# Kernel tuning notes

Measured on AMD Instinct MI355X. Metric: run time of the kernel, lower is better.

The kernel has to match this reference:

```python
import jax, jax.numpy as jnp
import numpy as np

TEMPERATURE = 0.07
HARD_NEG_WEIGHT = 0.5
MARGIN = 0.2
NUM_HARD_NEG = 3
BATCH = 8192
DIM = 256
NUM_CLASSES = 512


def setup_inputs() -> dict:
    key = jax.random.key(0)
    k1, k2 = jax.random.split(key)
    embeddings = jax.random.normal(k1, (BATCH, DIM), dtype=jnp.float32)
    labels = jax.random.randint(k2, (BATCH,), 0, NUM_CLASSES, dtype=jnp.int64)
    return {"embeddings": embeddings, "labels": labels}


def reference(embeddings, labels):
    B = embeddings.shape[0]
    dt = embeddings.dtype
    # L2 normalize (torch F.normalize with eps clamp)
    norm = jnp.maximum(jnp.linalg.norm(embeddings, axis=-1, keepdims=True), 1e-12)
    e = embeddings / norm
    sim = jnp.matmul(e, e.T) / TEMPERATURE  # [B, B]

    same = (labels[:, None] == labels[None, :]).astype(dt)
    eye = jnp.eye(B, dtype=dt)
    pos_mask = same - eye            # positives excluding self
    neg_mask = 1.0 - same            # negatives (diag is 0 since labels==labels)

    # basic InfoNCE-style loss (unnormalized exp, as in the original)
    exp_sim = jnp.exp(sim) * (1.0 - eye)
    pos_sim = (exp_sim * pos_mask).sum(axis=-1)
    all_sim = exp_sim.sum(axis=-1)
    basic = -jnp.log(pos_sim / (all_sim + 1e-10) + 1e-10)
    has_pos = pos_mask.sum(axis=-1) > 0
    hp = has_pos.astype(dt)
    n_hp = jnp.maximum(hp.sum(), 1.0)
    basic_loss = (basic * hp).sum() / n_hp

    # hard negative mining: top-k most similar negatives vs best positive
    neg_inf = -jnp.inf
    neg_sim = jnp.where(neg_mask > 0, sim, neg_inf)
    k = min(NUM_HARD_NEG, B - 1)
    hard_neg_mean = jax.lax.top_k(neg_sim, k)[0].mean(axis=-1)
    pos_max = jnp.where(pos_mask > 0, sim, neg_inf).max(axis=-1)
    h = jax.nn.relu(hard_neg_mean - pos_max + MARGIN)
    h = jnp.where(has_pos, h, 0.0)
    hard_loss = (h * hp).sum() / n_hp

    # margin ranking: max positive vs max negative
    max_neg = neg_sim.max(axis=-1)
    m = jax.nn.relu(max_neg - pos_max + MARGIN)
    valid = (pos_max > neg_inf) & (max_neg > neg_inf)
    v = valid.astype(dt)
    n_v = jnp.maximum(v.sum(), 1.0)
    margin_loss = jnp.where(v.sum() > 0, jnp.where(valid, m, 0.0).sum() / n_v, 0.0)

    total = basic_loss + HARD_NEG_WEIGHT * hard_loss + 0.1 * margin_loss
    return total
```

## Files before the change

kernel.cpp:

```cpp
#include <hip/hip_runtime.h>
#include <cstdint>
#include <cstddef>

#define BATCH  8192
#define DIM    256
#define NSTRIP 8
#define SCOLS  1024
#define MROWS  128
#define NTILE  64
#define NITER  (SCOLS/NTILE)

static constexpr float INV_T   = 1.0f / 0.07f;
static constexpr float EXP2_SC = 1.4426950408889634f / 0.07f;
static constexpr float MARGIN  = 0.2f;

typedef __attribute__((ext_vector_type(8))) short short8;
typedef __attribute__((ext_vector_type(4))) float f32x4;

__device__ __forceinline__ unsigned short f2bf(float f){
  unsigned int u = __float_as_uint(f);
  u += 0x7FFFu + ((u >> 16) & 1u);
  return (unsigned short)(u >> 16);
}

__device__ __forceinline__ void ins3(float& t0, float& t1, float& t2, float s){
  float m0 = fmaxf(t0, s); float r1 = fminf(t0, s); t0 = m0;
  float m1 = fmaxf(t1, r1); float r2 = fminf(t1, r1); t1 = m1;
  t2 = fmaxf(t2, r2);
}

__global__ void norm_cast_kernel(const float* __restrict__ emb,
                                 unsigned short* __restrict__ E,
                                 float* __restrict__ accum){
  if (blockIdx.x == 0 && threadIdx.x < 8) accum[threadIdx.x] = 0.0f;
  const int wave = threadIdx.x >> 6;
  const int lane = threadIdx.x & 63;
  const int row  = blockIdx.x * 4 + wave;
  const float4 v = *(const float4*)(emb + (size_t)row * DIM + lane * 4);
  float ss = v.x*v.x + v.y*v.y + v.z*v.z + v.w*v.w;
  #pragma unroll
  for (int m = 1; m < 64; m <<= 1) ss += __shfl_xor(ss, m, 64);
  float nrm = fmaxf(sqrtf(ss), 1e-12f);
  float inv = 1.0f / nrm;
  ushort4 o;
  o.x = f2bf(v.x * inv); o.y = f2bf(v.y * inv);
  o.z = f2bf(v.z * inv); o.w = f2bf(v.w * inv);
  *(ushort4*)(E + (size_t)row * DIM + lane * 4) = o;
}

__global__ __launch_bounds__(256, 2)
void sim_stats_kernel(const unsigned short* __restrict__ E,
                      const int* __restrict__ labels,
                      float* __restrict__ partials){
  const int strip = blockIdx.x;
  const int rb    = blockIdx.y * MROWS;
  const int cs    = strip * SCOLS;
  const int tid   = threadIdx.x;
  const int wave  = tid >> 6;
  const int lane  = tid & 63;
  const int l     = lane & 15;
  const int q     = lane >> 4;

  __shared__ short8 Bs[32 * 64];
  __shared__ int labs[SCOLS];

  for (int i = tid; i < SCOLS; i += 256) labs[i] = labels[cs + i];

  const int row0 = rb + wave * 32;

  short8 a[2][8];
  #pragma unroll
  for (int rt = 0; rt < 2; ++rt){
    const unsigned short* rp = E + (size_t)(row0 + rt*16 + l) * DIM + q * 8;
    #pragma unroll
    for (int kk = 0; kk < 8; ++kk)
      a[rt][kk] = *(const short8*)(rp + kk * 32);
  }

  int labr[2][4];
  #pragma unroll
  for (int rt = 0; rt < 2; ++rt)
    #pragma unroll
    for (int rr = 0; rr < 4; ++rr)
      labr[rt][rr] = labels[row0 + rt*16 + q*4 + rr];

  float all_s[8], pos_s[8], pos_m[8], t0[8], t1[8], t2[8];
  #pragma unroll
  for (int s = 0; s < 8; ++s){
    all_s[s] = 0.f; pos_s[s] = 0.f;
    pos_m[s] = -INFINITY; t0[s] = -INFINITY; t1[s] = -INFINITY; t2[s] = -INFINITY;
  }

  for (int it = 0; it < NITER; ++it){
    const int cb = cs + it * NTILE;
    __syncthreads();
    #pragma unroll
    for (int ci = 0; ci < 8; ++ci){
      const int c = wave * 8 + ci;
      const unsigned short* g = E + (size_t)(cb + lane) * DIM + c * 8;
      __builtin_amdgcn_global_load_lds(
        (const __attribute__((address_space(1))) unsigned int*)g,
        (__attribute__((address_space(3))) unsigned int*)&Bs[c * 64],
        16, 0, 0);
    }
    __syncthreads();

    #pragma unroll
    for (int t = 0; t < 4; ++t){
      const int gcol = cb + t * 16 + l;
      const int labc = labs[it * NTILE + t * 16 + l];
      f32x4 acc0 = {0.f,0.f,0.f,0.f};
      f32x4 acc1 = {0.f,0.f,0.f,0.f};
      #pragma unroll
      for (int kk = 0; kk < 8; ++kk){
        short8 b = Bs[(kk * 4 + q) * 64 + t * 16 + l];
        acc0 = __builtin_amdgcn_mfma_f32_16x16x32_bf16(a[0][kk], b, acc0, 0, 0, 0);
        acc1 = __builtin_amdgcn_mfma_f32_16x16x32_bf16(a[1][kk], b, acc1, 0, 0, 0);
      }
      #pragma unroll
      for (int rt = 0; rt < 2; ++rt){
        #pragma unroll
        for (int rr = 0; rr < 4; ++rr){
          const float d    = rt ? acc1[rr] : acc0[rr];
          const int   s    = rt * 4 + rr;
          const int   grow = row0 + rt * 16 + q * 4 + rr;
          const float sim  = d * INV_T;
          const float ex   = __builtin_amdgcn_exp2f(d * EXP2_SC);
          const bool same  = (labc == labr[rt][rr]);
          const bool self  = (gcol == grow);
          all_s[s] += self ? 0.f : ex;
          const bool ispos = same && !self;
          pos_s[s] += ispos ? ex : 0.f;
          pos_m[s]  = fmaxf(pos_m[s], ispos ? sim : -INFINITY);
          const float sn = same ? -INFINITY : sim;
          ins3(t0[s], t1[s], t2[s], sn);
        }
      }
    }
  }

  #pragma unroll
  for (int mask = 1; mask < 16; mask <<= 1){
    #pragma unroll
    for (int s = 0; s < 8; ++s){
      all_s[s] += __shfl_xor(all_s[s], mask, 64);
      pos_s[s] += __shfl_xor(pos_s[s], mask, 64);
      pos_m[s]  = fmaxf(pos_m[s], __shfl_xor(pos_m[s], mask, 64));
      float b0 = __shfl_xor(t0[s], mask, 64);
      float b1 = __shfl_xor(t1[s], mask, 64);
      float b2 = __shfl_xor(t2[s], mask, 64);
      ins3(t0[s], t1[s], t2[s], b0);
      ins3(t0[s], t1[s], t2[s], b1);
      ins3(t0[s], t1[s], t2[s], b2);
    }
  }

  if (l == 0){
    #pragma unroll
    for (int s = 0; s < 8; ++s){
      const int grow = row0 + (s >> 2) * 16 + q * 4 + (s & 3);
      float* p = partials + ((size_t)grow * NSTRIP + strip) * 6;
      p[0] = all_s[s]; p[1] = pos_s[s]; p[2] = pos_m[s];
      p[3] = t0[s];    p[4] = t1[s];    p[5] = t2[s];
    }
  }
}

__global__ void merge_kernel(const float* __restrict__ partials,
                             float* __restrict__ accum){
  const int row = blockIdx.x * 256 + threadIdx.x;
  float all_s = 0.f, pos_s = 0.f, pos_m = -INFINITY;
  float t0 = -INFINITY, t1 = -INFINITY, t2 = -INFINITY;
  #pragma unroll
  for (int s = 0; s < NSTRIP; ++s){
    const float* p = partials + ((size_t)row * NSTRIP + s) * 6;
    all_s += p[0]; pos_s += p[1];
    pos_m = fmaxf(pos_m, p[2]);
    ins3(t0, t1, t2, p[3]); ins3(t0, t1, t2, p[4]); ins3(t0, t1, t2, p[5]);
  }
  const bool has_pos = pos_m > -INFINITY;
  float vb = 0.f, vh = 0.f, vhp = 0.f, vm = 0.f, vv = 0.f;
  if (has_pos){
    vhp = 1.f;
    vb  = -logf(pos_s / (all_s + 1e-10f) + 1e-10f);
    const float hnm = (t0 + t1 + t2) * (1.f/3.f);
    vh  = fmaxf(hnm - pos_m + MARGIN, 0.f);
    if (t0 > -INFINITY){
      vv = 1.f;
      vm = fmaxf(t0 - pos_m + MARGIN, 0.f);
    }
  }
  float vals[5] = {vb, vh, vhp, vm, vv};
  #pragma unroll
  for (int m = 1; m < 64; m <<= 1)
    #pragma unroll
    for (int i = 0; i < 5; ++i) vals[i] += __shfl_xor(vals[i], m, 64);
  if ((threadIdx.x & 63) == 0){
    #pragma unroll
    for (int i = 0; i < 5; ++i) atomicAdd(&accum[i], vals[i]);
  }
}

__global__ void final_kernel(const float* __restrict__ accum,
                             float* __restrict__ out){
  if (threadIdx.x == 0){
    const float nhp   = fmaxf(accum[2], 1.f);
    const float basic = accum[0] / nhp;
    const float hard  = accum[1] / nhp;
    const float marg  = (accum[4] > 0.f) ? (accum[3] / fmaxf(accum[4], 1.f)) : 0.f;
    out[0] = basic + 0.5f * hard + 0.1f * marg;
  }
}

extern "C" void kernel_launch(void* const* d_in, const int* in_sizes, int n_in,
                              void* d_out, int out_size, void* d_ws, size_t ws_size,
                              hipStream_t stream){
  const float* emb  = (const float*)d_in[0];
  const int* labels = (const int*)d_in[1];
  float* out        = (float*)d_out;
  char* ws          = (char*)d_ws;

  unsigned short* E = (unsigned short*)ws;
  const size_t E_BYTES = (size_t)BATCH * DIM * 2;
  float* partials   = (float*)(ws + E_BYTES);
  const size_t P_BYTES = (size_t)BATCH * NSTRIP * 6 * sizeof(float);
  float* accum      = (float*)(ws + E_BYTES + P_BYTES);

  norm_cast_kernel<<<BATCH/4, 256, 0, stream>>>(emb, E, accum);
  sim_stats_kernel<<<dim3(NSTRIP, BATCH/MROWS), 256, 0, stream>>>(E, labels, partials);
  merge_kernel<<<BATCH/256, 256, 0, stream>>>(partials, accum);
  final_kernel<<<1, 64, 0, stream>>>(accum, out);
}
```

Baseline: 142.8 us.

## Double-buffer column tiles, specialize self tiles, use med3 top-k, fuse final reduction

The similarity kernel now uses narrower 512-column strips with 32-column tiles and double-buffered LDS staging, so the next tile's global-to-LDS load overlaps with compute. Occupancy is raised to 4 blocks per CU. The self-mask logic runs only on tiles that intersect the diagonal. The top-3 insertion uses v_med3, and statistics stay in log2-scaled units with a LN2 rescale in the merge step. The final kernel is folded into the merge kernel through a last-block atomic counter, which removes one launch but doubles the partials traffic.

```diff
diff --git a/kernel.cpp b/kernel.cpp
--- a/kernel.cpp
+++ b/kernel.cpp
@@ -4,14 +4,14 @@
 
 #define BATCH  8192
 #define DIM    256
-#define NSTRIP 8
-#define SCOLS  1024
+#define NSTRIP 16
+#define SCOLS  512
 #define MROWS  128
-#define NTILE  64
+#define NTILE  32
 #define NITER  (SCOLS/NTILE)
 
-static constexpr float INV_T   = 1.0f / 0.07f;
 static constexpr float EXP2_SC = 1.4426950408889634f / 0.07f;
+static constexpr float LN2     = 0.6931471805599453f;
 static constexpr float MARGIN  = 0.2f;
 
 typedef __attribute__((ext_vector_type(8))) short short8;
@@ -23,10 +23,17 @@
   return (unsigned short)(u >> 16);
 }
 
+__device__ __forceinline__ float med3f(float a, float b, float c){
+  float r;
+  asm("v_med3_f32 %0, %1, %2, %3" : "=v"(r) : "v"(a), "v"(b), "v"(c));
+  return r;
+}
+
 __device__ __forceinline__ void ins3(float& t0, float& t1, float& t2, float s){
-  float m0 = fmaxf(t0, s); float r1 = fminf(t0, s); t0 = m0;
-  float m1 = fmaxf(t1, r1); float r2 = fminf(t1, r1); t1 = m1;
-  t2 = fmaxf(t2, r2);
+  const float r1 = med3f(s, t0, t1);
+  const float r2 = med3f(s, t1, t2);
+  t0 = fmaxf(t0, s);
+  t1 = r1; t2 = r2;
 }
 
 __global__ void norm_cast_kernel(const float* __restrict__ emb,
@@ -48,7 +55,41 @@
   *(ushort4*)(E + (size_t)row * DIM + lane * 4) = o;
 }
 
-__global__ __launch_bounds__(256, 2)
+template<bool SELF>
+__device__ __forceinline__ void stats_update(
+    const f32x4& acc0, const f32x4& acc1,
+    const int labc, const int gcol, const int row0, const int q,
+    const int (&labr)[2][4],
+    float (&all_s)[8], float (&pos_s)[8], float (&pos_m)[8],
+    float (&t0)[8], float (&t1)[8], float (&t2)[8])
+{
+  #pragma unroll
+  for (int rt = 0; rt < 2; ++rt){
+    #pragma unroll
+    for (int rr = 0; rr < 4; ++rr){
+      const float d  = rt ? acc1[rr] : acc0[rr];
+      const int   s  = rt * 4 + rr;
+      const float z  = d * EXP2_SC;
+      const float ex = __builtin_amdgcn_exp2f(z);
+      const bool same = (labc == labr[rt][rr]);
+      bool  ispos = same;
+      float exa   = ex;
+      if (SELF){
+        const int grow = row0 + rt * 16 + q * 4 + rr;
+        const bool self = (gcol == grow);
+        ispos = same && !self;
+        exa   = self ? 0.f : ex;
+      }
+      all_s[s] += exa;
+      pos_s[s] += ispos ? ex : 0.f;
+      pos_m[s]  = fmaxf(pos_m[s], ispos ? z : -INFINITY);
+      const float sn = same ? -INFINITY : z;
+      ins3(t0[s], t1[s], t2[s], sn);
+    }
+  }
+}
+
+__global__ __launch_bounds__(256, 4)
 void sim_stats_kernel(const unsigned short* __restrict__ E,
                       const int* __restrict__ labels,
                       float* __restrict__ partials){
@@ -61,12 +102,29 @@
   const int l     = lane & 15;
   const int q     = lane >> 4;
 
-  __shared__ short8 Bs[32 * 64];
+  __shared__ short8 Bs0[32 * 32];
+  __shared__ short8 Bs1[32 * 32];
   __shared__ int labs[SCOLS];
 
   for (int i = tid; i < SCOLS; i += 256) labs[i] = labels[cs + i];
 
   const int row0 = rb + wave * 32;
+
+  auto stage = [&](short8* dst, int cb){
+    #pragma unroll
+    for (int i2 = 0; i2 < 4; ++i2){
+      const int cbase = wave * 8 + i2 * 2;
+      const int c = cbase + (lane >> 5);
+      const int r = lane & 31;
+      const unsigned short* g = E + (size_t)(cb + r) * DIM + c * 8;
+      __builtin_amdgcn_global_load_lds(
+        (const __attribute__((address_space(1))) unsigned int*)g,
+        (__attribute__((address_space(3))) unsigned int*)(dst + cbase * 32),
+        16, 0, 0);
+    }
+  };
+
+  stage(Bs0, cs);
 
   short8 a[2][8];
   #pragma unroll
@@ -91,52 +149,40 @@
     pos_m[s] = -INFINITY; t0[s] = -INFINITY; t1[s] = -INFINITY; t2[s] = -INFINITY;
   }
 
-  for (int it = 0; it < NITER; ++it){
+  auto compute = [&](const short8* B, int it){
     const int cb = cs + it * NTILE;
-    __syncthreads();
-    #pragma unroll
-    for (int ci = 0; ci < 8; ++ci){
-      const int c = wave * 8 + ci;
-      const unsigned short* g = E + (size_t)(cb + lane) * DIM + c * 8;
-      __builtin_amdgcn_global_load_lds(
-        (const __attribute__((address_space(1))) unsigned int*)g,
-        (__attribute__((address_space(3))) unsigned int*)&Bs[c * 64],
-        16, 0, 0);
-    }
-    __syncthreads();
-
-    #pragma unroll
-    for (int t = 0; t < 4; ++t){
-      const int gcol = cb + t * 16 + l;
+    #pragma unroll
+    for (int t = 0; t < 2; ++t){
+      const int c0   = cb + t * 16;
+      const int gcol = c0 + l;
       const int labc = labs[it * NTILE + t * 16 + l];
       f32x4 acc0 = {0.f,0.f,0.f,0.f};
       f32x4 acc1 = {0.f,0.f,0.f,0.f};
       #pragma unroll
       for (int kk = 0; kk < 8; ++kk){
-        short8 b = Bs[(kk * 4 + q) * 64 + t * 16 + l];
+        short8 b = B[(kk * 4 + q) * 32 + t * 16 + l];
         acc0 = __builtin_amdgcn_mfma_f32_16x16x32_bf16(a[0][kk], b, acc0, 0, 0, 0);
         acc1 = __builtin_amdgcn_mfma_f32_16x16x32_bf16(a[1][kk], b, acc1, 0, 0, 0);
       }
-      #pragma unroll
-      for (int rt = 0; rt < 2; ++rt){
-        #pragma unroll
-        for (int rr = 0; rr < 4; ++rr){
-          const float d    = rt ? acc1[rr] : acc0[rr];
-          const int   s    = rt * 4 + rr;
-          const int   grow = row0 + rt * 16 + q * 4 + rr;
-          const float sim  = d * INV_T;
-          const float ex   = __builtin_amdgcn_exp2f(d * EXP2_SC);
-          const bool same  = (labc == labr[rt][rr]);
-          const bool self  = (gcol == grow);
-          all_s[s] += self ? 0.f : ex;
-          const bool ispos = same && !self;
-          pos_s[s] += ispos ? ex : 0.f;
-          pos_m[s]  = fmaxf(pos_m[s], ispos ? sim : -INFINITY);
-          const float sn = same ? -INFINITY : sim;
-          ins3(t0[s], t1[s], t2[s], sn);
-        }
-      }
-    }
+      const bool selfT = (c0 < row0 + 32) && (row0 < c0 + 16);
+      if (selfT)
+        stats_update<true >(acc0, acc1, labc, gcol, row0, q, labr,
+                            all_s, pos_s, pos_m, t0, t1, t2);
+      else
+        stats_update<false>(acc0, acc1, labc, gcol, row0, q, labr,
+                            all_s, pos_s, pos_m, t0, t1, t2);
+    }
+  };
+
+  __syncthreads();
+
+  for (int it2 = 0; it2 < NITER; it2 += 2){
+    stage(Bs1, cs + (it2 + 1) * NTILE);
+    compute(Bs0, it2);
+    __syncthreads();
+    if (it2 + 2 < NITER) stage(Bs0, cs + (it2 + 2) * NTILE);
+    compute(Bs1, it2 + 1);
+    __syncthreads();
   }
 
   #pragma unroll
@@ -167,8 +213,9 @@
 }
 
 __global__ void merge_kernel(const float* __restrict__ partials,
-                             float* __restrict__ accum){
-  const int row = blockIdx.x * 256 + threadIdx.x;
+                             float* __restrict__ accum,
+                             float* __restrict__ out){
+  const int row = blockIdx.x * 64 + threadIdx.x;
   float all_s = 0.f, pos_s = 0.f, pos_m = -INFINITY;
   float t0 = -INFINITY, t1 = -INFINITY, t2 = -INFINITY;
   #pragma unroll
@@ -184,10 +231,10 @@
     vhp = 1.f;
     vb  = -logf(pos_s / (all_s + 1e-10f) + 1e-10f);
     const float hnm = (t0 + t1 + t2) * (1.f/3.f);
-    vh  = fmaxf(hnm - pos_m + MARGIN, 0.f);
+    vh  = fmaxf((hnm - pos_m) * LN2 + MARGIN, 0.f);
     if (t0 > -INFINITY){
       vv = 1.f;
-      vm = fmaxf(t0 - pos_m + MARGIN, 0.f);
+      vm = fmaxf((t0 - pos_m) * LN2 + MARGIN, 0.f);
     }
   }
   float vals[5] = {vb, vh, vhp, vm, vv};
@@ -195,20 +242,23 @@
   for (int m = 1; m < 64; m <<= 1)
     #pragma unroll
     for (int i = 0; i < 5; ++i) vals[i] += __shfl_xor(vals[i], m, 64);
-  if ((threadIdx.x & 63) == 0){
+  if (threadIdx.x == 0){
     #pragma unroll
     for (int i = 0; i < 5; ++i) atomicAdd(&accum[i], vals[i]);
-  }
-}
-
-__global__ void final_kernel(const float* __restrict__ accum,
-                             float* __restrict__ out){
-  if (threadIdx.x == 0){
-    const float nhp   = fmaxf(accum[2], 1.f);
-    const float basic = accum[0] / nhp;
-    const float hard  = accum[1] / nhp;
-    const float marg  = (accum[4] > 0.f) ? (accum[3] / fmaxf(accum[4], 1.f)) : 0.f;
-    out[0] = basic + 0.5f * hard + 0.1f * marg;
+    __threadfence();
+    const unsigned prev = atomicAdd((unsigned int*)&accum[7], 1u);
+    if (prev == (unsigned)(gridDim.x - 1)){
+      const float a0 = atomicAdd(&accum[0], 0.f);
+      const float a1 = atomicAdd(&accum[1], 0.f);
+      const float a2 = atomicAdd(&accum[2], 0.f);
+      const float a3 = atomicAdd(&accum[3], 0.f);
+      const float a4 = atomicAdd(&accum[4], 0.f);
+      const float nhp   = fmaxf(a2, 1.f);
+      const float basic = a0 / nhp;
+      const float hard  = a1 / nhp;
+      const float marg  = (a4 > 0.f) ? (a3 / fmaxf(a4, 1.f)) : 0.f;
+      out[0] = basic + 0.5f * hard + 0.1f * marg;
+    }
   }
 }
 
@@ -228,6 +278,5 @@
 
   norm_cast_kernel<<<BATCH/4, 256, 0, stream>>>(emb, E, accum);
   sim_stats_kernel<<<dim3(NSTRIP, BATCH/MROWS), 256, 0, stream>>>(E, labels, partials);
-  merge_kernel<<<BATCH/256, 256, 0, stream>>>(partials, accum);
-  final_kernel<<<1, 64, 0, stream>>>(accum, out);
-}
+  merge_kernel<<<BATCH/64, 64, 0, stream>>>(partials, accum, out);
+}
```

Measured after the change: 470.8 us. +229.6%, slower.
